# Kernel tuning notes

Hardware: AMD Instinct MI355X
Metric: run time of the kernel (lower is better)

Reference implementation:

```python
import jax, jax.numpy as jnp
import numpy as np

B, L, D = 16, 4096, 512


def setup_inputs() -> dict:
    key = jax.random.key(0)
    ks = jax.random.split(key, 8)
    s = 1.0 / np.sqrt(D)
    x = jax.random.normal(ks[0], (B, L, D), dtype=jnp.float32)
    Wk = jax.random.normal(ks[1], (D, D), dtype=jnp.float32) * s
    Wq = jax.random.normal(ks[2], (D, D), dtype=jnp.float32) * s
    Wv = jax.random.normal(ks[3], (D, D), dtype=jnp.float32) * s
    bk = jnp.zeros((D,), jnp.float32)
    bq = jnp.zeros((D,), jnp.float32)
    bv = jnp.zeros((D,), jnp.float32)
    lens = jax.random.randint(ks[4], (B,), 1, L + 1, dtype=jnp.int32)
    return {"x": x, "Wk": Wk, "bk": bk, "Wq": Wq, "bq": bq,
            "Wv": Wv, "bv": bv, "lens": lens}


def reference(x, Wk, bk, Wq, bq, Wv, bv, lens):
    # Dropout is identity in eval mode.
    x_k = jnp.tanh(jnp.einsum('bld,ed->ble', x, Wk) + bk)  # [B,L,D]
    x_q = jnp.tanh(jnp.einsum('bld,ed->ble', x, Wq) + bq)
    x_v = jnp.tanh(jnp.einsum('bld,ed->ble', x, Wv) + bv)
    # sum_j (x_k_i . x_q_j) == x_k_i . sum_j x_q_j  (algebraic collapse of the L x L bmm)
    q_sum = x_q.sum(axis=1)                                # [B,D]
    w = jnp.einsum('bld,bd->bl', x_k, q_sum) / (D ** 0.5)  # [B,L]
    pad = jnp.arange(L)[None, :] >= lens[:, None]          # True at padding
    w = jnp.where(pad, -jnp.inf, w)
    w = jax.nn.softmax(w, axis=1)                          # [B,L]
    # (x_v * w[...,None]).sum(-1) == x_v.sum(-1) * w
    return x_v.sum(axis=-1) * w                            # [B,L]
```

## Files before the change

### kernel.cpp

```cpp
#include <hip/hip_runtime.h>
#include <hip/hip_bf16.h>

typedef __attribute__((ext_vector_type(4)))  int   i32x4;
typedef __attribute__((ext_vector_type(16))) int   i32x16;
typedef __attribute__((ext_vector_type(16))) float f32x16;
typedef __attribute__((ext_vector_type(8)))  short short8;

#define SC1 (1.0f/4096.0f)
#define SC2 (1.0f/524288.0f)

static __device__ __forceinline__ float ftanh(float x) {
  float e = __builtin_amdgcn_exp2f(x * 2.885390081777927f);
  return 1.0f - 2.0f * __builtin_amdgcn_rcpf(e + 1.0f);
}
static __device__ __forceinline__ unsigned short bf16_rn(float f) {
  unsigned u = __float_as_uint(f);
  u += 0x7FFFu + ((u >> 16) & 1u);
  return (unsigned short)(u >> 16);
}
static __device__ __forceinline__ void quant2(float x, float sc, float inv, float losc,
                                              int& hi, int& lo) {
  float t  = __builtin_fmaf(x, sc, 12582912.0f);
  hi = __float_as_int(t) - 0x4B400000;
  float hf = t - 12582912.0f;
  float r  = __builtin_fmaf(hf, -inv, x);
  float t2 = __builtin_fmaf(r, losc, 12582912.0f);
  lo = __float_as_int(t2) - 0x4B400000;
}
static __device__ __forceinline__ void gll16(const void* g, void* l) {
  __builtin_amdgcn_global_load_lds((const __attribute__((address_space(1))) unsigned int*)g,
                                   (__attribute__((address_space(3))) unsigned int*)l, 16, 0, 0);
}
#define MFMA_I8(ACC, A, B) \
  asm("v_mfma_i32_32x32x32_i8 %0, %1, %2, %0" : "+v"(ACC) : "v"(A), "v"(B))

__global__ void prep_w(const float* __restrict__ Wq, const float* __restrict__ Wk,
                       const float* __restrict__ Wv,
                       char* __restrict__ B1, char* __restrict__ B2) {
  int gid = blockIdx.x * 256 + threadIdx.x;
  if (gid < 65536) {
    int chunk = gid >> 12, g = gid & 4095;
    char* dst = B1 + chunk * 65536 + g * 16;
    if (g < 2048) {
      int sel = g >> 10;
      int gg = g & 1023, nt = gg >> 6, lane = gg & 63;
      const float* src = Wq + (size_t)(nt * 32 + (lane & 31)) * 512 + chunk * 32 + (lane >> 5) * 16;
      union { char b[16]; i32x4 v; } ob;
#pragma unroll
      for (int j = 0; j < 16; ++j) {
        int h, l; quant2(src[j], 256.f, 1.f / 256.f, 32768.f, h, l);
        ob.b[j] = (char)(sel ? l : h);
      }
      *(i32x4*)dst = ob.v;
    } else {
      int gg = g - 2048, nt = gg >> 7, ks = (gg >> 6) & 1, lane = gg & 63;
      const float* src = Wv + (size_t)(nt * 32 + (lane & 31)) * 512 + chunk * 32 + ks * 16 + (lane >> 5) * 8;
      union { unsigned short s[8]; i32x4 v; } ob;
#pragma unroll
      for (int j = 0; j < 8; ++j) ob.s[j] = bf16_rn(src[j]);
      *(i32x4*)dst = ob.v;
    }
  } else {
    int gid2 = gid - 65536;
    int chunk = gid2 >> 11, g = gid2 & 2047;
    char* dst = B2 + chunk * 32768 + g * 16;
    int sel = g >> 10, gg = g & 1023, nt = gg >> 6, lane = gg & 63;
    const float* src = Wk + (size_t)(nt * 32 + (lane & 31)) * 512 + chunk * 32 + (lane >> 5) * 16;
    union { char b[16]; i32x4 v; } ob;
#pragma unroll
    for (int j = 0; j < 16; ++j) {
      int h, l; quant2(src[j], 256.f, 1.f / 256.f, 32768.f, h, l);
      ob.b[j] = (char)(sel ? l : h);
    }
    *(i32x4*)dst = ob.v;
  }
}

static __device__ __forceinline__ void stA8_32(char* Ab, int row, int d0, float4 xv) {
  int h0, l0, h1, l1, h2, l2, h3, l3;
  quant2(xv.x, 16.f, 0.0625f, 2048.f, h0, l0);
  quant2(xv.y, 16.f, 0.0625f, 2048.f, h1, l1);
  quant2(xv.z, 16.f, 0.0625f, 2048.f, h2, l2);
  quant2(xv.w, 16.f, 0.0625f, 2048.f, h3, l3);
  unsigned wh = (h0 & 255) | ((h1 & 255) << 8) | ((h2 & 255) << 16) | ((unsigned)(h3 & 255) << 24);
  unsigned wl = (l0 & 255) | ((l1 & 255) << 8) | ((l2 & 255) << 16) | ((unsigned)(l3 & 255) << 24);
  const int lane8 = (d0 >> 4) * 32 + row, j = d0 & 15;
  *(unsigned*)(Ab + lane8 * 16 + j) = wh;
  *(unsigned*)(Ab + 1024 + lane8 * 16 + j) = wl;
}
static __device__ __forceinline__ void stAv_32(char* Ab, int row, int d0, float4 xv) {
  unsigned long long b0 = bf16_rn(xv.x), b1 = bf16_rn(xv.y), b2 = bf16_rn(xv.z), b3 = bf16_rn(xv.w);
  unsigned long long vv = b0 | (b1 << 16) | (b2 << 32) | (b3 << 48);
  const int ks = d0 >> 4, rem = d0 & 15, hs8 = rem >> 3, j8 = rem & 7;
  *(unsigned long long*)(Ab + (ks * 64 + hs8 * 32 + row) * 16 + j8 * 2) = vv;
}

__global__ __launch_bounds__(512, 4) void pass_q(
    const float* __restrict__ x, const char* __restrict__ B1,
    const float* __restrict__ bq, float* __restrict__ qpart) {
  extern __shared__ char smem[];
  char* Bb0 = smem;          char* Bb1 = smem + 32768;
  char* Ab0 = smem + 65536;  char* Ab1 = smem + 67584;

  const int tid = threadIdx.x, lane = tid & 63, w = tid >> 6;
  const int l31 = lane & 31;
  const int tile = blockIdx.x;
  const int row = tid >> 3, d0 = (tid & 7) * 4;
  const float* gxr = x + ((size_t)tile * 32 + row) * 512 + d0;

  i32x16 q1[2] = {}, q2[2] = {};
  float4 xcur = {};

  if (tid < 256) { xcur = *(const float4*)(gxr); stA8_32(Ab0, row, d0, xcur); }
  {
    const char* src = B1 + tid * 16;
    char* dst = Bb0 + tid * 16;
#pragma unroll
    for (int i = 0; i < 4; ++i) gll16(src + i * 8192, dst + i * 8192);
  }
  if (tid < 256) xcur = *(const float4*)(gxr + 32);

#pragma unroll 1
  for (int c = 0; c < 16; ++c) {
    const int p = c & 1;
    char* Bc = p ? Bb1 : Bb0;  char* Bn = p ? Bb0 : Bb1;
    char* Ac = p ? Ab1 : Ab0;  char* An = p ? Ab0 : Ab1;
    __syncthreads();
    if (c < 15) {
      const char* src = B1 + (size_t)(c + 1) * 65536 + tid * 16;
      char* dst = Bn + tid * 16;
#pragma unroll
      for (int i = 0; i < 4; ++i) gll16(src + i * 8192, dst + i * 8192);
    }
    float4 xnext = xcur;
    if (tid < 256) {
      if (c < 14) xnext = *(const float4*)(gxr + (c + 2) * 32);
      if (c < 15) stA8_32(An, row, d0, xcur);
    }

    const int lo16 = lane * 16;
    i32x4 ah = *(const i32x4*)(Ac + lo16);
    i32x4 al = *(const i32x4*)(Ac + 1024 + lo16);
#pragma unroll
    for (int nn = 0; nn < 2; ++nn) {
      const int nt = w * 2 + nn;
      i32x4 bh = *(const i32x4*)(Bc + nt * 1024 + lo16);
      i32x4 bl = *(const i32x4*)(Bc + 16384 + nt * 1024 + lo16);
      MFMA_I8(q1[nn], ah, bh);
      MFMA_I8(q2[nn], ah, bl);
      MFMA_I8(q2[nn], al, bh);
    }
    xcur = xnext;
  }

#pragma unroll
  for (int nn = 0; nn < 2; ++nn) {
    const int col = (w * 2 + nn) * 32 + l31;
    const float bc = bq[col];
    float cs = 0.f;
#pragma unroll
    for (int r = 0; r < 16; ++r)
      cs += ftanh(__builtin_fmaf((float)q1[nn][r], SC1,
                  __builtin_fmaf((float)q2[nn][r], SC2, bc)));
    cs += __shfl_xor(cs, 32);
    if (lane < 32) qpart[(size_t)tile * 512 + col] = cs;
  }
}

__global__ __launch_bounds__(512, 4) void pass_v(
    const float* __restrict__ x, const char* __restrict__ B1,
    const float* __restrict__ bv, float* __restrict__ svout) {
  extern __shared__ char smem[];
  char* Bb0 = smem;          char* Bb1 = smem + 32768;
  char* Ab0 = smem + 65536;  char* Ab1 = smem + 67584;
  float* redv = (float*)(smem + 69632);

  const int tid = threadIdx.x, lane = tid & 63, w = tid >> 6;
  const int l31 = lane & 31, hs = lane >> 5;
  const int tile = blockIdx.x;
  const int row = tid >> 3, d0 = (tid & 7) * 4;
  const float* gxr = x + ((size_t)tile * 32 + row) * 512 + d0;

  f32x16 accv[2] = {};
  float4 xcur = {};

  if (tid < 256) { xcur = *(const float4*)(gxr); stAv_32(Ab0, row, d0, xcur); }
  {
    const char* src = B1 + 32768 + tid * 16;
    char* dst = Bb0 + tid * 16;
#pragma unroll
    for (int i = 0; i < 4; ++i) gll16(src + i * 8192, dst + i * 8192);
  }
  if (tid < 256) xcur = *(const float4*)(gxr + 32);

#pragma unroll 1
  for (int c = 0; c < 16; ++c) {
    const int p = c & 1;
    char* Bc = p ? Bb1 : Bb0;  char* Bn = p ? Bb0 : Bb1;
    char* Ac = p ? Ab1 : Ab0;  char* An = p ? Ab0 : Ab1;
    __syncthreads();
    if (c < 15) {
      const char* src = B1 + (size_t)(c + 1) * 65536 + 32768 + tid * 16;
      char* dst = Bn + tid * 16;
#pragma unroll
      for (int i = 0; i < 4; ++i) gll16(src + i * 8192, dst + i * 8192);
    }
    float4 xnext = xcur;
    if (tid < 256) {
      if (c < 14) xnext = *(const float4*)(gxr + (c + 2) * 32);
      if (c < 15) stAv_32(An, row, d0, xcur);
    }

    const int lo16 = lane * 16;
#pragma unroll
    for (int ks = 0; ks < 2; ++ks) {
      short8 av = *(const short8*)(Ac + ks * 1024 + lo16);
#pragma unroll
      for (int nn = 0; nn < 2; ++nn) {
        const int nt = w * 2 + nn;
        short8 bvf = *(const short8*)(Bc + (nt * 2 + ks) * 1024 + lo16);
        accv[nn] = __builtin_amdgcn_mfma_f32_32x32x16_bf16(av, bvf, accv[nn], 0, 0, 0);
      }
    }
    xcur = xnext;
  }

  const float bv0 = bv[(w * 2 + 0) * 32 + l31];
  const float bv1 = bv[(w * 2 + 1) * 32 + l31];
  __syncthreads();
#pragma unroll
  for (int r = 0; r < 16; ++r) {
    float s = ftanh(accv[0][r] + bv0) + ftanh(accv[1][r] + bv1);
#pragma unroll
    for (int off = 1; off <= 16; off <<= 1) s += __shfl_xor(s, off);
    if (l31 == 0) redv[w * 32 + (r & 3) + 8 * (r >> 2) + 4 * hs] = s;
  }
  __syncthreads();
  if (tid < 32) {
    float s = 0.f;
#pragma unroll
    for (int j = 0; j < 8; ++j) s += redv[j * 32 + tid];
    svout[(size_t)tile * 32 + tid] = s;
  }
}

__global__ __launch_bounds__(512, 4) void pass_k(
    const float* __restrict__ x, const char* __restrict__ B2,
    const float* __restrict__ bk, const float* __restrict__ q_sum,
    float* __restrict__ scores) {
  extern __shared__ char smem[];
  char* Bb0 = smem;          char* Bb1 = smem + 32768;
  char* Ab0 = smem + 65536;  char* Ab1 = smem + 67584;
  float* redk = (float*)(smem + 69632);

  const int tid = threadIdx.x, lane = tid & 63, w = tid >> 6;
  const int l31 = lane & 31, hs = lane >> 5;
  const int tile = blockIdx.x;
  const int row = tid >> 3, d0 = (tid & 7) * 4;
  const float* gxr = x + ((size_t)tile * 32 + row) * 512 + d0;

  i32x16 k1[2] = {}, k2[2] = {};
  float4 xcur = {};

  if (tid < 256) { xcur = *(const float4*)(gxr); stA8_32(Ab0, row, d0, xcur); }
  {
    const char* src = B2 + tid * 16;
    char* dst = Bb0 + tid * 16;
#pragma unroll
    for (int i = 0; i < 4; ++i) gll16(src + i * 8192, dst + i * 8192);
  }
  if (tid < 256) xcur = *(const float4*)(gxr + 32);

#pragma unroll 1
  for (int c = 0; c < 16; ++c) {
    const int p = c & 1;
    char* Bc = p ? Bb1 : Bb0;  char* Bn = p ? Bb0 : Bb1;
    char* Ac = p ? Ab1 : Ab0;  char* An = p ? Ab0 : Ab1;
    __syncthreads();
    if (c < 15) {
      const char* src = B2 + (size_t)(c + 1) * 32768 + tid * 16;
      char* dst = Bn + tid * 16;
#pragma unroll
      for (int i = 0; i < 4; ++i) gll16(src + i * 8192, dst + i * 8192);
    }
    float4 xnext = xcur;
    if (tid < 256) {
      if (c < 14) xnext = *(const float4*)(gxr + (c + 2) * 32);
      if (c < 15) stA8_32(An, row, d0, xcur);
    }

    const int lo16 = lane * 16;
    i32x4 ah = *(const i32x4*)(Ac + lo16);
    i32x4 al = *(const i32x4*)(Ac + 1024 + lo16);
#pragma unroll
    for (int nn = 0; nn < 2; ++nn) {
      const int nt = w * 2 + nn;
      i32x4 bh = *(const i32x4*)(Bc + nt * 1024 + lo16);
      i32x4 bl = *(const i32x4*)(Bc + 16384 + nt * 1024 + lo16);
      MFMA_I8(k1[nn], ah, bh);
      MFMA_I8(k2[nn], ah, bl);
      MFMA_I8(k2[nn], al, bh);
    }
    xcur = xnext;
  }

  const int b = tile >> 7;
  const int c0 = (w * 2 + 0) * 32 + l31, c1 = (w * 2 + 1) * 32 + l31;
  const float qs0 = q_sum[b * 512 + c0], qs1 = q_sum[b * 512 + c1];
  const float bk0 = bk[c0], bk1 = bk[c1];
  __syncthreads();
#pragma unroll
  for (int r = 0; r < 16; ++r) {
    float p0 = __builtin_fmaf((float)k1[0][r], SC1,
               __builtin_fmaf((float)k2[0][r], SC2, bk0));
    float p1 = __builtin_fmaf((float)k1[1][r], SC1,
               __builtin_fmaf((float)k2[1][r], SC2, bk1));
    float s = ftanh(p0) * qs0 + ftanh(p1) * qs1;
#pragma unroll
    for (int off = 1; off <= 16; off <<= 1) s += __shfl_xor(s, off);
    if (l31 == 0) redk[w * 32 + (r & 3) + 8 * (r >> 2) + 4 * hs] = s;
  }
  __syncthreads();
  if (tid < 32) {
    float s = 0.f;
#pragma unroll
    for (int j = 0; j < 8; ++j) s += redk[j * 32 + tid];
    scores[(size_t)tile * 32 + tid] = s;
  }
}

__global__ void reduce_q(const float* __restrict__ qpart, float* __restrict__ q_sum) {
  int b = blockIdx.x, e = threadIdx.x;
  const float* p = qpart + (size_t)b * 128 * 512 + e;
  float s = 0.f;
#pragma unroll 4
  for (int j = 0; j < 128; ++j) s += p[j * 512];
  q_sum[b * 512 + e] = s;
}

__global__ void softmax_out(const float* __restrict__ scores,
                            const float* __restrict__ sv,
                            const int* __restrict__ lens,
                            float* __restrict__ out) {
  const int b = blockIdx.x, tid = threadIdx.x;
  const int lane = tid & 63, wid = tid >> 6;
  const int len = lens[b];
  const float scale = 0.04419417382415922f;
  __shared__ float sb[4], sb2[4];

  float sreg[16];
  const float* sc = scores + (size_t)b * 4096;
#pragma unroll
  for (int j = 0; j < 16; ++j) sreg[j] = sc[tid + j * 256] * scale;

  float m = -1e30f;
#pragma unroll
  for (int j = 0; j < 16; ++j)
    if (tid + j * 256 < len) m = fmaxf(m, sreg[j]);
#pragma unroll
  for (int off = 32; off >= 1; off >>= 1) m = fmaxf(m, __shfl_xor(m, off));
  if (lane == 0) sb[wid] = m;
  __syncthreads();
  m = fmaxf(fmaxf(sb[0], sb[1]), fmaxf(sb[2], sb[3]));

  float s = 0.f;
#pragma unroll
  for (int j = 0; j < 16; ++j)
    if (tid + j * 256 < len) s += expf(sreg[j] - m);
#pragma unroll
  for (int off = 32; off >= 1; off >>= 1) s += __shfl_xor(s, off);
  if (lane == 0) sb2[wid] = s;
  __syncthreads();
  const float inv = 1.f / (sb2[0] + sb2[1] + sb2[2] + sb2[3]);

  const float* svb = sv + (size_t)b * 4096;
  float* ob = out + (size_t)b * 4096;
#pragma unroll
  for (int j = 0; j < 16; ++j) {
    int l = tid + j * 256;
    ob[l] = (l < len) ? svb[l] * expf(sreg[j] - m) * inv : 0.0f;
  }
}

extern "C" void kernel_launch(void* const* d_in, const int* in_sizes, int n_in,
                              void* d_out, int out_size, void* d_ws, size_t ws_size,
                              hipStream_t stream) {
  const float* x  = (const float*)d_in[0];
  const float* Wk = (const float*)d_in[1];
  const float* bk = (const float*)d_in[2];
  const float* Wq = (const float*)d_in[3];
  const float* bq = (const float*)d_in[4];
  const float* Wv = (const float*)d_in[5];
  const float* bv = (const float*)d_in[6];
  const int* lens = (const int*)d_in[7];
  float* out = (float*)d_out;

  char* ws = (char*)d_ws;
  char*  B1     = ws;
  char*  B2     = ws + 1048576;
  float* qpart  = (float*)(ws + 1572864);
  float* q_sum  = (float*)(ws + 5767168);
  float* svbuf  = (float*)(ws + 5799936);
  float* scores = (float*)(ws + 6062080);

  prep_w<<<384, 256, 0, stream>>>(Wq, Wk, Wv, B1, B2);
  pass_q<<<2048, 512, 69632, stream>>>(x, B1, bq, qpart);
  pass_v<<<2048, 512, 70656, stream>>>(x, B1, bv, svbuf);
  reduce_q<<<16, 512, 0, stream>>>(qpart, q_sum);
  pass_k<<<2048, 512, 70656, stream>>>(x, B2, bk, q_sum, scores);
  softmax_out<<<16, 256, 0, stream>>>(scores, svbuf, lens, out);
}
```

Measured before the change: 263.5 us.

## Double row tile to 64 per block and stagger K-chunk order across blocks

Each block now processes 64 rows with 1024 threads (two M-tiles of 32 sharing each staged weight chunk), halving the number of weight chunk loads into LDS per row. The K-chunk iteration order is rotated per block by tile&15 so concurrent blocks read different weight slices, spreading L2/memory traffic. pass_q now reduces its two M-tiles in LDS before writing partial sums, halving qpart size and the reduce_q loop. Larger blocks raise LDS per block and may limit occupancy.

```diff
diff --git a/kernel.cpp b/kernel.cpp
--- a/kernel.cpp
+++ b/kernel.cpp
@@ -76,7 +76,8 @@
   }
 }
 
-static __device__ __forceinline__ void stA8_32(char* Ab, int row, int d0, float4 xv) {
+static __device__ __forceinline__ void stageAi8(char* Ab, int row, int d0, float4 xv) {
+  const int mt = row >> 5, l31 = row & 31;
   int h0, l0, h1, l1, h2, l2, h3, l3;
   quant2(xv.x, 16.f, 0.0625f, 2048.f, h0, l0);
   quant2(xv.y, 16.f, 0.0625f, 2048.f, h1, l1);
@@ -84,41 +85,44 @@
   quant2(xv.w, 16.f, 0.0625f, 2048.f, h3, l3);
   unsigned wh = (h0 & 255) | ((h1 & 255) << 8) | ((h2 & 255) << 16) | ((unsigned)(h3 & 255) << 24);
   unsigned wl = (l0 & 255) | ((l1 & 255) << 8) | ((l2 & 255) << 16) | ((unsigned)(l3 & 255) << 24);
-  const int lane8 = (d0 >> 4) * 32 + row, j = d0 & 15;
-  *(unsigned*)(Ab + lane8 * 16 + j) = wh;
-  *(unsigned*)(Ab + 1024 + lane8 * 16 + j) = wl;
-}
-static __device__ __forceinline__ void stAv_32(char* Ab, int row, int d0, float4 xv) {
+  const int lane8 = (d0 >> 4) * 32 + l31, j = d0 & 15;
+  *(unsigned*)(Ab + (mt * 64 + lane8) * 16 + j) = wh;
+  *(unsigned*)(Ab + 2048 + (mt * 64 + lane8) * 16 + j) = wl;
+}
+static __device__ __forceinline__ void stageAv(char* Ab, int row, int d0, float4 xv) {
+  const int mt = row >> 5, l31 = row & 31;
   unsigned long long b0 = bf16_rn(xv.x), b1 = bf16_rn(xv.y), b2 = bf16_rn(xv.z), b3 = bf16_rn(xv.w);
   unsigned long long vv = b0 | (b1 << 16) | (b2 << 32) | (b3 << 48);
   const int ks = d0 >> 4, rem = d0 & 15, hs8 = rem >> 3, j8 = rem & 7;
-  *(unsigned long long*)(Ab + (ks * 64 + hs8 * 32 + row) * 16 + j8 * 2) = vv;
-}
-
-__global__ __launch_bounds__(512, 4) void pass_q(
+  *(unsigned long long*)(Ab + ((mt * 2 + ks) * 64 + hs8 * 32 + l31) * 16 + j8 * 2) = vv;
+}
+
+__global__ __launch_bounds__(1024, 4) void pass_q(
     const float* __restrict__ x, const char* __restrict__ B1,
     const float* __restrict__ bq, float* __restrict__ qpart) {
   extern __shared__ char smem[];
   char* Bb0 = smem;          char* Bb1 = smem + 32768;
-  char* Ab0 = smem + 65536;  char* Ab1 = smem + 67584;
+  char* Ab0 = smem + 65536;  char* Ab1 = smem + 69632;
+  float* redq = (float*)(smem + 73728);
 
   const int tid = threadIdx.x, lane = tid & 63, w = tid >> 6;
   const int l31 = lane & 31;
+  const int mt = w >> 3, ng = w & 7;
   const int tile = blockIdx.x;
+  const int stag = tile & 15;
   const int row = tid >> 3, d0 = (tid & 7) * 4;
-  const float* gxr = x + ((size_t)tile * 32 + row) * 512 + d0;
+  const float* gxr = x + ((size_t)tile * 64 + row) * 512 + d0;
 
   i32x16 q1[2] = {}, q2[2] = {};
   float4 xcur = {};
 
-  if (tid < 256) { xcur = *(const float4*)(gxr); stA8_32(Ab0, row, d0, xcur); }
+  if (tid < 512) { xcur = *(const float4*)(gxr + stag * 32); stageAi8(Ab0, row, d0, xcur); }
   {
-    const char* src = B1 + tid * 16;
-    char* dst = Bb0 + tid * 16;
-#pragma unroll
-    for (int i = 0; i < 4; ++i) gll16(src + i * 8192, dst + i * 8192);
-  }
-  if (tid < 256) xcur = *(const float4*)(gxr + 32);
+    const char* src = B1 + (size_t)stag * 65536 + tid * 16;
+    gll16(src, Bb0 + tid * 16);
+    gll16(src + 16384, Bb0 + 16384 + tid * 16);
+  }
+  if (tid < 512) xcur = *(const float4*)(gxr + (((stag + 1) & 15)) * 32);
 
 #pragma unroll 1
   for (int c = 0; c < 16; ++c) {
@@ -127,23 +131,22 @@
     char* Ac = p ? Ab1 : Ab0;  char* An = p ? Ab0 : Ab1;
     __syncthreads();
     if (c < 15) {
-      const char* src = B1 + (size_t)(c + 1) * 65536 + tid * 16;
-      char* dst = Bn + tid * 16;
-#pragma unroll
-      for (int i = 0; i < 4; ++i) gll16(src + i * 8192, dst + i * 8192);
+      const char* src = B1 + (size_t)(((c + 1 + stag) & 15)) * 65536 + tid * 16;
+      gll16(src, Bn + tid * 16);
+      gll16(src + 16384, Bn + 16384 + tid * 16);
     }
     float4 xnext = xcur;
-    if (tid < 256) {
-      if (c < 14) xnext = *(const float4*)(gxr + (c + 2) * 32);
-      if (c < 15) stA8_32(An, row, d0, xcur);
+    if (tid < 512) {
+      if (c < 14) xnext = *(const float4*)(gxr + (((c + 2 + stag) & 15)) * 32);
+      if (c < 15) stageAi8(An, row, d0, xcur);
     }
 
     const int lo16 = lane * 16;
-    i32x4 ah = *(const i32x4*)(Ac + lo16);
-    i32x4 al = *(const i32x4*)(Ac + 1024 + lo16);
+    i32x4 ah = *(const i32x4*)(Ac + mt * 1024 + lo16);
+    i32x4 al = *(const i32x4*)(Ac + 2048 + mt * 1024 + lo16);
 #pragma unroll
     for (int nn = 0; nn < 2; ++nn) {
-      const int nt = w * 2 + nn;
+      const int nt = ng * 2 + nn;
       i32x4 bh = *(const i32x4*)(Bc + nt * 1024 + lo16);
       i32x4 bl = *(const i32x4*)(Bc + 16384 + nt * 1024 + lo16);
       MFMA_I8(q1[nn], ah, bh);
@@ -155,7 +158,7 @@
 
 #pragma unroll
   for (int nn = 0; nn < 2; ++nn) {
-    const int col = (w * 2 + nn) * 32 + l31;
+    const int col = (ng * 2 + nn) * 32 + l31;
     const float bc = bq[col];
     float cs = 0.f;
 #pragma unroll
@@ -163,35 +166,38 @@
       cs += ftanh(__builtin_fmaf((float)q1[nn][r], SC1,
                   __builtin_fmaf((float)q2[nn][r], SC2, bc)));
     cs += __shfl_xor(cs, 32);
-    if (lane < 32) qpart[(size_t)tile * 512 + col] = cs;
-  }
-}
-
-__global__ __launch_bounds__(512, 4) void pass_v(
+    if (lane < 32) redq[mt * 512 + col] = cs;
+  }
+  __syncthreads();
+  if (tid < 512) qpart[(size_t)tile * 512 + tid] = redq[tid] + redq[512 + tid];
+}
+
+__global__ __launch_bounds__(1024, 4) void pass_v(
     const float* __restrict__ x, const char* __restrict__ B1,
     const float* __restrict__ bv, float* __restrict__ svout) {
   extern __shared__ char smem[];
   char* Bb0 = smem;          char* Bb1 = smem + 32768;
-  char* Ab0 = smem + 65536;  char* Ab1 = smem + 67584;
-  float* redv = (float*)(smem + 69632);
+  char* Ab0 = smem + 65536;  char* Ab1 = smem + 69632;
+  float* redv = (float*)(smem + 73728);
 
   const int tid = threadIdx.x, lane = tid & 63, w = tid >> 6;
   const int l31 = lane & 31, hs = lane >> 5;
+  const int mt = w >> 3, ng = w & 7;
   const int tile = blockIdx.x;
+  const int stag = tile & 15;
   const int row = tid >> 3, d0 = (tid & 7) * 4;
-  const float* gxr = x + ((size_t)tile * 32 + row) * 512 + d0;
+  const float* gxr = x + ((size_t)tile * 64 + row) * 512 + d0;
 
   f32x16 accv[2] = {};
   float4 xcur = {};
 
-  if (tid < 256) { xcur = *(const float4*)(gxr); stAv_32(Ab0, row, d0, xcur); }
+  if (tid < 512) { xcur = *(const float4*)(gxr + stag * 32); stageAv(Ab0, row, d0, xcur); }
   {
-    const char* src = B1 + 32768 + tid * 16;
-    char* dst = Bb0 + tid * 16;
-#pragma unroll
-    for (int i = 0; i < 4; ++i) gll16(src + i * 8192, dst + i * 8192);
-  }
-  if (tid < 256) xcur = *(const float4*)(gxr + 32);
+    const char* src = B1 + (size_t)stag * 65536 + 32768 + tid * 16;
+    gll16(src, Bb0 + tid * 16);
+    gll16(src + 16384, Bb0 + 16384 + tid * 16);
+  }
+  if (tid < 512) xcur = *(const float4*)(gxr + (((stag + 1) & 15)) * 32);
 
 #pragma unroll 1
   for (int c = 0; c < 16; ++c) {
@@ -200,24 +206,23 @@
     char* Ac = p ? Ab1 : Ab0;  char* An = p ? Ab0 : Ab1;
     __syncthreads();
     if (c < 15) {
-      const char* src = B1 + (size_t)(c + 1) * 65536 + 32768 + tid * 16;
-      char* dst = Bn + tid * 16;
-#pragma unroll
-      for (int i = 0; i < 4; ++i) gll16(src + i * 8192, dst + i * 8192);
+      const char* src = B1 + (size_t)(((c + 1 + stag) & 15)) * 65536 + 32768 + tid * 16;
+      gll16(src, Bn + tid * 16);
+      gll16(src + 16384, Bn + 16384 + tid * 16);
     }
     float4 xnext = xcur;
-    if (tid < 256) {
-      if (c < 14) xnext = *(const float4*)(gxr + (c + 2) * 32);
-      if (c < 15) stAv_32(An, row, d0, xcur);
+    if (tid < 512) {
+      if (c < 14) xnext = *(const float4*)(gxr + (((c + 2 + stag) & 15)) * 32);
+      if (c < 15) stageAv(An, row, d0, xcur);
     }
 
     const int lo16 = lane * 16;
 #pragma unroll
     for (int ks = 0; ks < 2; ++ks) {
-      short8 av = *(const short8*)(Ac + ks * 1024 + lo16);
+      short8 av = *(const short8*)(Ac + (mt * 2 + ks) * 1024 + lo16);
 #pragma unroll
       for (int nn = 0; nn < 2; ++nn) {
-        const int nt = w * 2 + nn;
+        const int nt = ng * 2 + nn;
         short8 bvf = *(const short8*)(Bc + (nt * 2 + ks) * 1024 + lo16);
         accv[nn] = __builtin_amdgcn_mfma_f32_32x32x16_bf16(av, bvf, accv[nn], 0, 0, 0);
       }
@@ -225,51 +230,52 @@
     xcur = xnext;
   }
 
-  const float bv0 = bv[(w * 2 + 0) * 32 + l31];
-  const float bv1 = bv[(w * 2 + 1) * 32 + l31];
+  const float bv0 = bv[(ng * 2 + 0) * 32 + l31];
+  const float bv1 = bv[(ng * 2 + 1) * 32 + l31];
   __syncthreads();
 #pragma unroll
   for (int r = 0; r < 16; ++r) {
     float s = ftanh(accv[0][r] + bv0) + ftanh(accv[1][r] + bv1);
 #pragma unroll
     for (int off = 1; off <= 16; off <<= 1) s += __shfl_xor(s, off);
-    if (l31 == 0) redv[w * 32 + (r & 3) + 8 * (r >> 2) + 4 * hs] = s;
-  }
-  __syncthreads();
-  if (tid < 32) {
+    if (l31 == 0) redv[ng * 64 + mt * 32 + (r & 3) + 8 * (r >> 2) + 4 * hs] = s;
+  }
+  __syncthreads();
+  if (tid < 64) {
     float s = 0.f;
 #pragma unroll
-    for (int j = 0; j < 8; ++j) s += redv[j * 32 + tid];
-    svout[(size_t)tile * 32 + tid] = s;
-  }
-}
-
-__global__ __launch_bounds__(512, 4) void pass_k(
+    for (int j = 0; j < 8; ++j) s += redv[j * 64 + tid];
+    svout[(size_t)tile * 64 + tid] = s;
+  }
+}
+
+__global__ __launch_bounds__(1024, 4) void pass_k(
     const float* __restrict__ x, const char* __restrict__ B2,
     const float* __restrict__ bk, const float* __restrict__ q_sum,
     float* __restrict__ scores) {
   extern __shared__ char smem[];
   char* Bb0 = smem;          char* Bb1 = smem + 32768;
-  char* Ab0 = smem + 65536;  char* Ab1 = smem + 67584;
-  float* redk = (float*)(smem + 69632);
+  char* Ab0 = smem + 65536;  char* Ab1 = smem + 69632;
+  float* redk = (float*)(smem + 73728);
 
   const int tid = threadIdx.x, lane = tid & 63, w = tid >> 6;
   const int l31 = lane & 31, hs = lane >> 5;
+  const int mt = w >> 3, ng = w & 7;
   const int tile = blockIdx.x;
+  const int stag = tile & 15;
   const int row = tid >> 3, d0 = (tid & 7) * 4;
-  const float* gxr = x + ((size_t)tile * 32 + row) * 512 + d0;
+  const float* gxr = x + ((size_t)tile * 64 + row) * 512 + d0;
 
   i32x16 k1[2] = {}, k2[2] = {};
   float4 xcur = {};
 
-  if (tid < 256) { xcur = *(const float4*)(gxr); stA8_32(Ab0, row, d0, xcur); }
+  if (tid < 512) { xcur = *(const float4*)(gxr + stag * 32); stageAi8(Ab0, row, d0, xcur); }
   {
-    const char* src = B2 + tid * 16;
-    char* dst = Bb0 + tid * 16;
-#pragma unroll
-    for (int i = 0; i < 4; ++i) gll16(src + i * 8192, dst + i * 8192);
-  }
-  if (tid < 256) xcur = *(const float4*)(gxr + 32);
+    const char* src = B2 + (size_t)stag * 32768 + tid * 16;
+    gll16(src, Bb0 + tid * 16);
+    gll16(src + 16384, Bb0 + 16384 + tid * 16);
+  }
+  if (tid < 512) xcur = *(const float4*)(gxr + (((stag + 1) & 15)) * 32);
 
 #pragma unroll 1
   for (int c = 0; c < 16; ++c) {
@@ -278,23 +284,22 @@
     char* Ac = p ? Ab1 : Ab0;  char* An = p ? Ab0 : Ab1;
     __syncthreads();
     if (c < 15) {
-      const char* src = B2 + (size_t)(c + 1) * 32768 + tid * 16;
-      char* dst = Bn + tid * 16;
-#pragma unroll
-      for (int i = 0; i < 4; ++i) gll16(src + i * 8192, dst + i * 8192);
+      const char* src = B2 + (size_t)(((c + 1 + stag) & 15)) * 32768 + tid * 16;
+      gll16(src, Bn + tid * 16);
+      gll16(src + 16384, Bn + 16384 + tid * 16);
     }
     float4 xnext = xcur;
-    if (tid < 256) {
-      if (c < 14) xnext = *(const float4*)(gxr + (c + 2) * 32);
-      if (c < 15) stA8_32(An, row, d0, xcur);
+    if (tid < 512) {
+      if (c < 14) xnext = *(const float4*)(gxr + (((c + 2 + stag) & 15)) * 32);
+      if (c < 15) stageAi8(An, row, d0, xcur);
     }
 
     const int lo16 = lane * 16;
-    i32x4 ah = *(const i32x4*)(Ac + lo16);
-    i32x4 al = *(const i32x4*)(Ac + 1024 + lo16);
+    i32x4 ah = *(const i32x4*)(Ac + mt * 1024 + lo16);
+    i32x4 al = *(const i32x4*)(Ac + 2048 + mt * 1024 + lo16);
 #pragma unroll
     for (int nn = 0; nn < 2; ++nn) {
-      const int nt = w * 2 + nn;
+      const int nt = ng * 2 + nn;
       i32x4 bh = *(const i32x4*)(Bc + nt * 1024 + lo16);
       i32x4 bl = *(const i32x4*)(Bc + 16384 + nt * 1024 + lo16);
       MFMA_I8(k1[nn], ah, bh);
@@ -304,8 +309,8 @@
     xcur = xnext;
   }
 
-  const int b = tile >> 7;
-  const int c0 = (w * 2 + 0) * 32 + l31, c1 = (w * 2 + 1) * 32 + l31;
+  const int b = tile >> 6;
+  const int c0 = (ng * 2 + 0) * 32 + l31, c1 = (ng * 2 + 1) * 32 + l31;
   const float qs0 = q_sum[b * 512 + c0], qs1 = q_sum[b * 512 + c1];
   const float bk0 = bk[c0], bk1 = bk[c1];
   __syncthreads();
@@ -318,23 +323,23 @@
     float s = ftanh(p0) * qs0 + ftanh(p1) * qs1;
 #pragma unroll
     for (int off = 1; off <= 16; off <<= 1) s += __shfl_xor(s, off);
-    if (l31 == 0) redk[w * 32 + (r & 3) + 8 * (r >> 2) + 4 * hs] = s;
-  }
-  __syncthreads();
-  if (tid < 32) {
+    if (l31 == 0) redk[ng * 64 + mt * 32 + (r & 3) + 8 * (r >> 2) + 4 * hs] = s;
+  }
+  __syncthreads();
+  if (tid < 64) {
     float s = 0.f;
 #pragma unroll
-    for (int j = 0; j < 8; ++j) s += redk[j * 32 + tid];
-    scores[(size_t)tile * 32 + tid] = s;
+    for (int j = 0; j < 8; ++j) s += redk[j * 64 + tid];
+    scores[(size_t)tile * 64 + tid] = s;
   }
 }
 
 __global__ void reduce_q(const float* __restrict__ qpart, float* __restrict__ q_sum) {
   int b = blockIdx.x, e = threadIdx.x;
-  const float* p = qpart + (size_t)b * 128 * 512 + e;
+  const float* p = qpart + (size_t)b * 64 * 512 + e;
   float s = 0.f;
 #pragma unroll 4
-  for (int j = 0; j < 128; ++j) s += p[j * 512];
+  for (int j = 0; j < 64; ++j) s += p[j * 512];
   q_sum[b * 512 + e] = s;
 }
 
@@ -399,14 +404,14 @@
   char*  B1     = ws;
   char*  B2     = ws + 1048576;
   float* qpart  = (float*)(ws + 1572864);
-  float* q_sum  = (float*)(ws + 5767168);
-  float* svbuf  = (float*)(ws + 5799936);
-  float* scores = (float*)(ws + 6062080);
+  float* q_sum  = (float*)(ws + 3670016);
+  float* svbuf  = (float*)(ws + 3702784);
+  float* scores = (float*)(ws + 3964928);
 
   prep_w<<<384, 256, 0, stream>>>(Wq, Wk, Wv, B1, B2);
-  pass_q<<<2048, 512, 69632, stream>>>(x, B1, bq, qpart);
-  pass_v<<<2048, 512, 70656, stream>>>(x, B1, bv, svbuf);
+  pass_q<<<1024, 1024, 77824, stream>>>(x, B1, bq, qpart);
+  pass_v<<<1024, 1024, 75776, stream>>>(x, B1, bv, svbuf);
   reduce_q<<<16, 512, 0, stream>>>(qpart, q_sum);
-  pass_k<<<2048, 512, 70656, stream>>>(x, B2, bk, q_sum, scores);
+  pass_k<<<1024, 1024, 75776, stream>>>(x, B2, bk, q_sum, scores);
   softmax_out<<<16, 256, 0, stream>>>(scores, svbuf, lens, out);
 }
```

Result: faster. 235.3 us (-10.7%).
